# Kernel optimization log

Hardware: AMD Instinct MI355X
Metric: run time of the kernel (lower is better)

The kernel has to match this reference:

```python
import jax, jax.numpy as jnp
import numpy as np

# --- constants from init_kwargs / globals in source ---
HIDDEN = 512
SAMPLE_RATE = 22050
HOP_LENGTH = 256
MAX_DURATION = 10
MIN_DURATION = 1
TARGET_FRAMES = SAMPLE_RATE * MAX_DURATION // HOP_LENGTH  # 861
B, T = 64, 512


def setup_inputs() -> dict:
    key = jax.random.key(0)
    k1, k2 = jax.random.split(key)
    batch = jax.random.normal(k1, (B, T, HIDDEN), dtype=jnp.float32)
    predicted_durations = jax.random.uniform(
        k2, (B, T, 1), dtype=jnp.float32, minval=0.0, maxval=float(MAX_DURATION))
    return {"batch": batch, "predicted_durations": predicted_durations}


def reference(batch, predicted_durations):
    # [B, T] integer per-token frame counts
    d = jnp.round(jnp.clip(predicted_durations, MIN_DURATION, MAX_DURATION))
    d = d.astype(jnp.int32)[..., 0]
    ends = jnp.cumsum(d, axis=1)          # [B, T] exclusive end offset of each token
    total = ends[:, -1]                   # [B] total expanded frames per example
    frames = jnp.arange(TARGET_FRAMES, dtype=jnp.int32)  # [L]
    # For output frame j, source token = first token whose cumulative end > j.
    idx = jax.vmap(lambda e: jnp.searchsorted(e, frames, side='right'))(ends)  # [B, L]
    idx_c = jnp.minimum(idx, batch.shape[1] - 1)
    out = jnp.take_along_axis(batch, idx_c[..., None], axis=1)  # [B, L, H]
    # Frames past the total expanded length are zero-padding; truncation to
    # TARGET_FRAMES is implicit since we only materialize L frames.
    valid = (frames[None, :] < total[:, None]).astype(batch.dtype)  # [B, L]
    return out * valid[..., None]
```

## Files before the change

### kernel.cpp

```cpp
#include <hip/hip_runtime.h>

#define NB 64
#define NT 512
#define HIDDEN 512
#define TF 861
#define CHUNKS 32
#define FPC 27
#define GRID (NB * CHUNKS)

__global__ __launch_bounds__(256) void lr_fused(const float* __restrict__ pred,
                                                const float4* __restrict__ batch4,
                                                float4* __restrict__ out4) {
    __shared__ int wsum[4];
    __shared__ int sidx[FPC];

    const int bid = blockIdx.x;
    const int sid = (bid & 7) * (GRID >> 3) + (bid >> 3);
    const int b = sid >> 5;
    const int chunk = sid & 31;
    const int base = chunk * FPC;

    const int t = threadIdx.x;
    const int lane = t & 63;
    const int wid = t >> 6;

    float2 p2 = ((const float2*)(pred + b * NT))[t];
    int d0 = (int)rintf(fminf(fmaxf(p2.x, 1.f), 10.f));
    int d1 = (int)rintf(fminf(fmaxf(p2.y, 1.f), 10.f));
    int x = d0 + d1;
    #pragma unroll
    for (int off = 1; off < 64; off <<= 1) {
        int y = __shfl_up(x, off, 64);
        if (lane >= off) x += y;
    }
    if (lane == 63) wsum[wid] = x;
    if (t < FPC) sidx[t] = -1;
    __syncthreads();
    int prefix = 0;
    #pragma unroll
    for (int w = 0; w < 3; ++w)
        if (w < wid) prefix += wsum[w];
    x += prefix;

    const int end1   = x;
    const int start1 = x - d1;
    const int start0 = start1 - d0;
    const int wend = min(base + FPC, TF);
    {
        int lo = max(start0, base), hi = min(start1, wend);
        for (int f = lo; f < hi; ++f) sidx[f - base] = 2 * t;
        lo = max(start1, base); hi = min(end1, wend);
        for (int f = lo; f < hi; ++f) sidx[f - base] = 2 * t + 1;
    }
    __syncthreads();

    const float4* srcb = batch4 + ((size_t)b << 16);
    #pragma unroll 2
    for (int fo = wid; fo < FPC; fo += 4) {
        const int f = base + fo;
        if (f >= TF) break;
        const int idx = sidx[fo];
        float4 v0 = make_float4(0.f, 0.f, 0.f, 0.f);
        float4 v1 = v0;
        if (idx >= 0) {
            const float4* src = srcb + ((size_t)idx << 7);
            v0 = src[lane];
            v1 = src[lane + 64];
        }
        float4* dst = out4 + (((size_t)b * TF + f) << 7);
        dst[lane] = v0;
        dst[lane + 64] = v1;
    }
}

extern "C" void kernel_launch(void* const* d_in, const int* in_sizes, int n_in,
                              void* d_out, int out_size, void* d_ws, size_t ws_size,
                              hipStream_t stream) {
    const float* batch = (const float*)d_in[0];
    const float* pred  = (const float*)d_in[1];
    float* out = (float*)d_out;

    lr_fused<<<GRID, 256, 0, stream>>>(pred, (const float4*)batch, (float4*)out);
}
```

Measured before the change: 27.11 us.

## Assign contiguous frame runs per wave, reuse loaded rows, nontemporal stores

Each wave now handles a contiguous run of 7 frames instead of a strided set, so it loads a source row only when the token index changes and reuses the registers for repeated frames. Output writes use nontemporal stores to avoid polluting cache with the large write-only output. Since durations average about 5.5 frames, most frames become register copies rather than reloads. The fixed 4x7 split covers 28 slots for 27 frames, so one wave gets 6 frames while the others get 7, and the serial dependency inside the unrolled steps may reduce memory-level parallelism.

```diff
diff --git a/kernel.cpp b/kernel.cpp
--- a/kernel.cpp
+++ b/kernel.cpp
@@ -8,11 +8,13 @@
 #define FPC 27
 #define GRID (NB * CHUNKS)
 
+typedef float v4f __attribute__((ext_vector_type(4)));
+
 __global__ __launch_bounds__(256) void lr_fused(const float* __restrict__ pred,
-                                                const float4* __restrict__ batch4,
-                                                float4* __restrict__ out4) {
+                                                const v4f* __restrict__ batch4,
+                                                v4f* __restrict__ out4) {
     __shared__ int wsum[4];
-    __shared__ int sidx[FPC];
+    __shared__ int sidx[28];
 
     const int bid = blockIdx.x;
     const int sid = (bid & 7) * (GRID >> 3) + (bid >> 3);
@@ -34,7 +36,7 @@
         if (lane >= off) x += y;
     }
     if (lane == 63) wsum[wid] = x;
-    if (t < FPC) sidx[t] = -1;
+    if (t < 28) sidx[t] = -1;
     __syncthreads();
     int prefix = 0;
     #pragma unroll
@@ -54,23 +56,38 @@
     }
     __syncthreads();
 
-    const float4* srcb = batch4 + ((size_t)b << 16);
-    #pragma unroll 2
-    for (int fo = wid; fo < FPC; fo += 4) {
-        const int f = base + fo;
-        if (f >= TF) break;
-        const int idx = sidx[fo];
-        float4 v0 = make_float4(0.f, 0.f, 0.f, 0.f);
-        float4 v1 = v0;
-        if (idx >= 0) {
-            const float4* src = srcb + ((size_t)idx << 7);
-            v0 = src[lane];
-            v1 = src[lane + 64];
-        }
-        float4* dst = out4 + (((size_t)b * TF + f) << 7);
-        dst[lane] = v0;
-        dst[lane + 64] = v1;
+    const int nv = wend - base;
+    const int run0 = wid * 7;
+    const v4f* srcb = batch4 + ((size_t)b << 16);
+    v4f* dstb = out4 + (((size_t)b * TF + base) << 7);
+
+    const int i0 = sidx[run0 + 0], i1 = sidx[run0 + 1], i2 = sidx[run0 + 2],
+              i3 = sidx[run0 + 3], i4 = sidx[run0 + 4], i5 = sidx[run0 + 5],
+              i6 = sidx[run0 + 6];
+
+    int curidx = -2;
+    v4f v0 = (v4f)(0.f), v1 = (v4f)(0.f);
+
+#define STEP(K, IK)                                                     \
+    if (run0 + (K) < nv) {                                              \
+        if ((IK) != curidx) {                                           \
+            curidx = (IK);                                              \
+            if ((IK) >= 0) {                                            \
+                const v4f* src = srcb + ((size_t)(IK) << 7);            \
+                v0 = src[lane];                                         \
+                v1 = src[lane + 64];                                    \
+            } else {                                                    \
+                v0 = (v4f)(0.f); v1 = (v4f)(0.f);                       \
+            }                                                           \
+        }                                                               \
+        v4f* dst = dstb + ((size_t)(run0 + (K)) << 7);                  \
+        __builtin_nontemporal_store(v0, dst + lane);                    \
+        __builtin_nontemporal_store(v1, dst + lane + 64);               \
     }
+
+    STEP(0, i0) STEP(1, i1) STEP(2, i2) STEP(3, i3)
+    STEP(4, i4) STEP(5, i5) STEP(6, i6)
+#undef STEP
 }
 
 extern "C" void kernel_launch(void* const* d_in, const int* in_sizes, int n_in,
@@ -80,5 +97,5 @@
     const float* pred  = (const float*)d_in[1];
     float* out = (float*)d_out;
 
-    lr_fused<<<GRID, 256, 0, stream>>>(pred, (const float4*)batch, (float4*)out);
+    lr_fused<<<GRID, 256, 0, stream>>>(pred, (const v4f*)batch, (v4f*)out);
 }
```

New measurement: 27.23 us. No clear change (+0.4%).
